# Kernel tuning notes

Measured on AMD Instinct MI355X. Metric: run time of the kernel, lower is better.

## Reference

```python
import jax, jax.numpy as jnp
import numpy as np

K = 60           # output_size (num tags)
START_TAG = 58
STOP_TAG = 59
NEG = -10000.0


def _conv1d(x, w, b, pad):
    # x: (B, Cin, T), w: (Cout, Cin, k) -> (B, Cout, T)
    y = jax.lax.conv_general_dilated(x, w, (1,), [(pad, pad)],
                                     dimension_numbers=('NCH', 'OIH', 'NCH'))
    return y + b[None, :, None]


def _cnn_feats(sentence, w1, b1, w2, b2, w3, b3, w4, b4, w5, b5, fc_w, fc_b):
    # sentence: (T, B, 3) -> (B, 3, T)
    x = jnp.transpose(sentence, (1, 2, 0))
    in2 = jax.nn.relu(_conv1d(x, w1, b1, 1))
    in3 = jax.nn.relu(_conv1d(in2, w2, b2, 1))
    in4 = jax.nn.relu(_conv1d(in3 + in2, w3, b3, 1))
    in5 = jax.nn.relu(_conv1d(in4 + in3, w4, b4, 1))
    c5 = jax.nn.relu(_conv1d(in5 + in4, w5, b5, 2))
    h = jnp.transpose(c5, (2, 0, 1))                 # (T, B, H)
    return jnp.einsum('tbh,kh->tbk', h, fc_w) + fc_b  # (T, B, K)


def _viterbi(feats, trans):
    Bsz = feats.shape[1]
    fv0 = jnp.full((Bsz, K), NEG, dtype=feats.dtype).at[:, START_TAG].set(0.0)

    def step(fv, feat):
        # scores[b, next, prev] = fv[b, prev] + trans[next, prev]
        scores = fv[:, None, :] + trans[None, :, :]
        bptr = jnp.argmax(scores, axis=2)             # (B, K)
        fv_new = jnp.max(scores, axis=2) + feat       # (B, K)
        return fv_new, bptr

    fv, bptrs = jax.lax.scan(step, fv0, feats)        # bptrs: (T, B, K)
    terminal = fv + trans[STOP_TAG]                   # (B, K)
    path_score = jnp.max(terminal, axis=1)            # (B,)
    best_last = jnp.argmax(terminal, axis=1)          # (B,)

    def back(tag, bp):
        prev = jnp.take_along_axis(bp, tag[:, None], axis=1)[:, 0]
        return prev, tag

    _, best_path = jax.lax.scan(back, best_last, bptrs, reverse=True)  # (T, B)
    return path_score, best_path


def setup_inputs() -> dict:
    key = jax.random.key(0)
    ks = jax.random.split(key, 14)
    T, B, HID = 8192, 2, 512

    def u(k, shape, fan_in):
        bound = 1.0 / np.sqrt(fan_in).astype(np.float32)
        return jax.random.uniform(k, shape, minval=-bound, maxval=bound, dtype=jnp.float32)

    sentence = jax.random.normal(ks[0], (T, B, 3), dtype=jnp.float32)
    w1 = u(ks[1], (HID, 3, 3), 3 * 3);      b1 = u(ks[2], (HID,), 3 * 3)
    w2 = u(ks[3], (HID, HID, 3), HID * 3);  b2 = u(ks[4], (HID,), HID * 3)
    w3 = u(ks[5], (HID, HID, 3), HID * 3);  b3 = u(ks[6], (HID,), HID * 3)
    w4 = u(ks[7], (HID, HID, 3), HID * 3);  b4 = u(ks[8], (HID,), HID * 3)
    w5 = u(ks[9], (HID, HID, 5), HID * 5);  b5 = u(ks[10], (HID,), HID * 5)
    fc_w = u(ks[11], (K, HID), HID);        fc_b = u(ks[12], (K,), HID)

    trans = jax.random.normal(ks[13], (K, K), dtype=jnp.float32)
    m = np.zeros((K, K), dtype=bool)
    m[START_TAG, :] = True
    m[:, STOP_TAG] = True
    for i in range(2, K):
        for j in range(2, K):
            if j <= i or j >= i + 2:
                m[j, i] = True
    trans = jnp.where(jnp.asarray(m), jnp.float32(NEG), trans)

    return {'sentence': sentence,
            'w1': w1, 'b1': b1, 'w2': w2, 'b2': b2, 'w3': w3, 'b3': b3,
            'w4': w4, 'b4': b4, 'w5': w5, 'b5': b5,
            'fc_w': fc_w, 'fc_b': fc_b, 'trans': trans}


def reference(sentence, w1, b1, w2, b2, w3, b3, w4, b4, w5, b5, fc_w, fc_b, trans):
    feats = _cnn_feats(sentence, w1, b1, w2, b2, w3, b3, w4, b4, w5, b5, fc_w, fc_b)
    path_score, best_path = _viterbi(feats, trans)
    return path_score, best_path
```

## Files before the change

### kernel.cpp

```cpp
#include <hip/hip_runtime.h>

#define BATCH 2
#define HID 512
#define KTAGS 60
#define NEGV -10000.0f
#define NINF -3.0e38f

template<int CTRL>
__device__ __forceinline__ float dmax(float x) {
    int r = __builtin_amdgcn_update_dpp(__float_as_int(x), __float_as_int(x),
                                        CTRL, 0xf, 0xf, false);
    return fmaxf(x, __int_as_float(r));
}
template<int CTRL>
__device__ __forceinline__ float dmov(float x, float old) {
    int r = __builtin_amdgcn_update_dpp(__float_as_int(old), __float_as_int(x),
                                        CTRL, 0xf, 0xf, false);
    return __int_as_float(r);
}
__device__ __forceinline__ float bfly16max(float x) {
    x = dmax<0xB1>(x);
    x = dmax<0x4E>(x);
    x = dmax<0x141>(x);
    x = dmax<0x140>(x);
    return x;
}

__global__ __launch_bounds__(256) void conv1_kernel(
    const float* __restrict__ sent, const float* __restrict__ w1,
    const float* __restrict__ b1, float* __restrict__ y, int T, int B)
{
    int t = blockIdx.x * 256 + threadIdx.x;
    int c = blockIdx.y;
    int b = blockIdx.z;
    if (t >= T) return;
    float acc = b1[c];
#pragma unroll
    for (int dk = 0; dk < 3; ++dk) {
        int tt = t + dk - 1;
        if (tt >= 0 && tt < T) {
#pragma unroll
            for (int ci = 0; ci < 3; ++ci)
                acc += sent[(size_t)tt * (B * 3) + b * 3 + ci] * w1[c * 9 + ci * 3 + dk];
        }
    }
    y[((size_t)b * HID + c) * T + t] = fmaxf(acc, 0.f);
}

__global__ __launch_bounds__(256) void wtrans_kernel(
    const float* __restrict__ w, float* __restrict__ wt, int K)
{
    int idx = blockIdx.x * 256 + threadIdx.x;
    int total = HID * HID * K;
    if (idx >= total) return;
    int co = idx / (HID * K);
    int rem = idx % (HID * K);
    int ci = rem / K, dk = rem % K;
    wt[((size_t)ci * K + dk) * HID + co] = w[idx];
}

template<int KTAP, bool RES>
__global__ __launch_bounds__(256) void conv_kernel(
    const float* __restrict__ x1, const float* __restrict__ x2,
    const float* __restrict__ wt, const float* __restrict__ bias,
    float* __restrict__ y, int T)
{
    const int PAD = KTAP / 2;
    const int t0 = blockIdx.x * 64;
    const int co0 = blockIdx.y * 128;
    const int b = blockIdx.z;
    __shared__ float Xs[16][72];
    __shared__ float Ws[16][KTAP][128];
    const int tid = threadIdx.x;
    const int tx = tid & 15;
    const int ty = tid >> 4;
    float acc[8][4] = {};
    const size_t plane = (size_t)HID * T;
    const float* xa = x1 + (size_t)b * plane;
    const float* xb = RES ? (x2 + (size_t)b * plane) : nullptr;

    float xr[5];
    float4 wr[2 * KTAP];
    int xci[5], xtt[5];
#pragma unroll
    for (int k = 0; k < 5; ++k) {
        int i = tid + k * 256;
        xci[k] = i / 68;
        xtt[k] = i % 68;
    }

    auto load_stage = [&](int c0) {
#pragma unroll
        for (int k = 0; k < 5; ++k) {
            float v = 0.f;
            if (tid + k * 256 < 16 * 68) {
                int t = t0 + xtt[k] - 2;
                if (t >= 0 && t < T) {
                    size_t off = (size_t)(c0 + xci[k]) * T + t;
                    v = xa[off];
                    if (RES) v += xb[off];
                }
            }
            xr[k] = v;
        }
#pragma unroll
        for (int k = 0; k < 2 * KTAP; ++k) {
            int i = tid + k * 256;
            int c4 = i & 31, r = i >> 5;
            int dk = r % KTAP, ci = r / KTAP;
            wr[k] = *(const float4*)&wt[(((size_t)(c0 + ci) * KTAP + dk) * HID) + co0 + c4 * 4];
        }
    };
    auto write_stage = [&]() {
#pragma unroll
        for (int k = 0; k < 5; ++k)
            if (tid + k * 256 < 16 * 68) Xs[xci[k]][xtt[k]] = xr[k];
#pragma unroll
        for (int k = 0; k < 2 * KTAP; ++k) {
            int i = tid + k * 256;
            int c4 = i & 31, r = i >> 5;
            int dk = r % KTAP, ci = r / KTAP;
            *(float4*)&Ws[ci][dk][c4 * 4] = wr[k];
        }
    };

    load_stage(0);
    for (int c0 = 0; c0 < HID; c0 += 16) {
        write_stage();
        __syncthreads();
        if (c0 + 16 < HID) load_stage(c0 + 16);
#pragma unroll 4
        for (int ci = 0; ci < 16; ++ci) {
            float f8[8];
            *(float4*)&f8[0] = *(const float4*)&Xs[ci][tx * 4];
            *(float4*)&f8[4] = *(const float4*)&Xs[ci][tx * 4 + 4];
#pragma unroll
            for (int dk = 0; dk < KTAP; ++dk) {
                float wv[8];
                *(float4*)&wv[0] = *(const float4*)&Ws[ci][dk][ty * 8];
                *(float4*)&wv[4] = *(const float4*)&Ws[ci][dk][ty * 8 + 4];
#pragma unroll
                for (int r = 0; r < 8; ++r)
#pragma unroll
                    for (int c = 0; c < 4; ++c)
                        acc[r][c] = fmaf(wv[r], f8[c + dk + (2 - PAD)], acc[r][c]);
            }
        }
        __syncthreads();
    }
#pragma unroll
    for (int r = 0; r < 8; ++r) {
        int co = co0 + ty * 8 + r;
        float bv = bias[co];
#pragma unroll
        for (int c = 0; c < 4; ++c) {
            int t = t0 + tx * 4 + c;
            float v = acc[r][c] + bv;
            y[(size_t)b * plane + (size_t)co * T + t] = fmaxf(v, 0.f);
        }
    }
}

__global__ __launch_bounds__(256) void fc_kernel(
    const float* __restrict__ x, const float* __restrict__ fw,
    const float* __restrict__ fb, float* __restrict__ feats, int T)
{
    int t0 = blockIdx.x * 64, b = blockIdx.y;
    __shared__ float Xs[64][65];
    __shared__ float Ws[64][60];
    int tid = threadIdx.x;
    int k = tid & 63, tq = tid >> 6;
    float acc[16] = {};
    const float* xb = x + (size_t)b * HID * T;
    for (int c0 = 0; c0 < HID; c0 += 64) {
        for (int i = tid; i < 64 * 64; i += 256) {
            int ci = i >> 6, tt = i & 63;
            Xs[ci][tt] = xb[(size_t)(c0 + ci) * T + t0 + tt];
        }
        for (int i = tid; i < 64 * 60; i += 256) {
            int kk = i % 60, ci = i / 60;
            Ws[ci][kk] = fw[(size_t)kk * HID + c0 + ci];
        }
        __syncthreads();
        if (k < KTAGS) {
#pragma unroll 8
            for (int ci = 0; ci < 64; ++ci) {
                float wv = Ws[ci][k];
#pragma unroll
                for (int i = 0; i < 16; ++i)
                    acc[i] = fmaf(wv, Xs[ci][tq * 16 + i], acc[i]);
            }
        }
        __syncthreads();
    }
    float bv = (k < KTAGS) ? fb[k] : 0.f;
#pragma unroll
    for (int i = 0; i < 16; ++i) {
        int t = t0 + tq * 16 + i;
        feats[((size_t)t * 2 + b) * 64 + k] = (k < KTAGS) ? acc[i] + bv : NINF;
    }
}

__global__ __launch_bounds__(64) void viterbi_fwd(
    const float* __restrict__ feats, const float* __restrict__ trans,
    float* __restrict__ fvbuf, int T)
{
    const int b = blockIdx.x;
    const int l = threadIdx.x;
    if (l >= 16) return;
    float tc0[4], tc1[4], trc[4], tr0[4], tr1[4], fv[4];
#pragma unroll
    for (int j = 0; j < 4; ++j) {
        int k = 4 * l + j;
        int kc = (k < KTAGS) ? k : (KTAGS - 1);
        bool real = (k < KTAGS);
        tc0[j] = trans[kc * KTAGS + 0];
        tc1[j] = trans[kc * KTAGS + 1];
        trc[j] = (kc >= 1) ? trans[kc * KTAGS + (kc - 1)] : NINF;
        tr0[j] = real ? trans[0 * KTAGS + kc] : NINF;
        tr1[j] = real ? trans[1 * KTAGS + kc] : NINF;
        fv[j]  = real ? ((k == 58) ? 0.f : NEGV) : NINF;
    }
    float fv0h = NEGV, fv1h = NEGV;
    {
        float4 st = {fv[0], fv[1], fv[2], fv[3]};
        *(float4*)&fvbuf[(size_t)b * 64 + 4 * l] = st;
    }
    const float* fp   = feats + b * 64 + 4 * l;
    const float* fp01 = feats + b * 64;
    float* fvp = fvbuf + 128 + b * 64 + 4 * l;

    auto step = [&](float4 f, float2 f01, int j, float* outp) {
        float a0 = fmaxf(fmaxf(fv[0] + tr0[0], fv[1] + tr0[1]), fmaxf(fv[2] + tr0[2], fv[3] + tr0[3]));
        float a1 = fmaxf(fmaxf(fv[0] + tr1[0], fv[1] + tr1[1]), fmaxf(fv[2] + tr1[2], fv[3] + tr1[3]));
        float hi = fmaxf(fv[2], fv[3]);
        float m2 = (l == 0) ? hi : fmaxf(fmaxf(fv[0], fv[1]), hi);
        a0 = bfly16max(a0);
        a1 = bfly16max(a1);
        m2 = bfly16max(m2);
        float p3 = dmov<0x111>(fv[3], fv[3]);
        float bulk = m2 + NEGV;
        float nf0 = a0 + f01.x;
        float nf1 = a1 + f01.y;
        float g0 = fmaxf(fmaxf(fv0h + tc0[0], fv1h + tc1[0]), fmaxf(p3    + trc[0], bulk)) + f.x;
        float g1 = fmaxf(fmaxf(fv0h + tc0[1], fv1h + tc1[1]), fmaxf(fv[0] + trc[1], bulk)) + f.y;
        float g2 = fmaxf(fmaxf(fv0h + tc0[2], fv1h + tc1[2]), fmaxf(fv[1] + trc[2], bulk)) + f.z;
        float g3 = fmaxf(fmaxf(fv0h + tc0[3], fv1h + tc1[3]), fmaxf(fv[2] + trc[3], bulk)) + f.w;
        fv[0] = (l == 0) ? nf0 : g0;
        fv[1] = (l == 0) ? nf1 : g1;
        fv[2] = g2;
        fv[3] = g3;
        fv0h = nf0; fv1h = nf1;
        float4 st = {fv[0], fv[1], fv[2], fv[3]};
        *(float4*)&outp[j * 128] = st;
    };

    float4 fr[8];
    float2 fr2[8];
#pragma unroll
    for (int j = 0; j < 8; ++j) {
        fr[j]  = *(const float4*)&fp[j * 128];
        fr2[j] = *(const float2*)&fp01[j * 128];
    }
    fp += 8 * 128; fp01 += 8 * 128;

    for (int t = 0; t < T; t += 8) {
#pragma unroll
        for (int j = 0; j < 8; ++j) {
            step(fr[j], fr2[j], j, fvp);
            fr[j]  = *(const float4*)&fp[j * 128];
            fr2[j] = *(const float2*)&fp01[j * 128];
        }
        fp += 8 * 128; fp01 += 8 * 128;
        fvp += 8 * 128;
    }
}

__global__ __launch_bounds__(256) void bptr_kernel(
    const float* __restrict__ fvbuf, const float* __restrict__ trans,
    unsigned char* __restrict__ bp, int T)
{
    int b = blockIdx.y;
    int t0 = blockIdx.x * 16;
    __shared__ float trT[KTAGS][64];
    __shared__ float fvs[16][64];
    int tid = threadIdx.x;
    for (int i = tid; i < KTAGS * 64; i += 256) {
        int p = i >> 6, nx = i & 63;
        trT[p][nx] = (nx < KTAGS) ? trans[(size_t)nx * KTAGS + p] : NINF;
    }
    for (int i = tid; i < 16 * 64; i += 256) {
        int w = i >> 6, lx = i & 63;
        fvs[w][lx] = fvbuf[((size_t)(t0 + w) * 2 + b) * 64 + lx];
    }
    __syncthreads();
    int nx = tid & 63, w0 = tid >> 6;
    if (nx < KTAGS) {
#pragma unroll
        for (int j = 0; j < 4; ++j) {
            int w = w0 * 4 + j;
            float m = NINF; int am = 0;
            for (int p = 0; p < KTAGS; ++p) {
                float s = fvs[w][p] + trT[p][nx];
                if (s > m) { m = s; am = p; }
            }
            bp[((size_t)(t0 + w) * 2 + b) * 64 + nx] = (unsigned char)am;
        }
    }
}

__global__ __launch_bounds__(64) void vit_chunkmap(
    const unsigned char* __restrict__ bp, unsigned char* __restrict__ cmap)
{
    int c = blockIdx.x, b = blockIdx.y;
    __shared__ unsigned char bl[128][64];
    int tid = threadIdx.x;
    const unsigned int* src = (const unsigned int*)bp;
    for (int i = tid; i < 128 * 16; i += 64) {
        int row = i >> 4, q = i & 15;
        ((unsigned int*)&bl[row][0])[q] = src[((size_t)(c * 128 + row) * 2 + b) * 16 + q];
    }
    __syncthreads();
    if (tid < KTAGS) {
        int tag = tid;
#pragma unroll 1
        for (int i = 127; i >= 0; --i) tag = bl[i][tag];
        cmap[(c * 2 + b) * 64 + tid] = (unsigned char)tag;
    }
}

__global__ void vit_boundary(const unsigned char* __restrict__ cmap,
                             const float* __restrict__ fvbuf,
                             const float* __restrict__ trans,
                             int* __restrict__ xbound, float* __restrict__ out,
                             int nch, int T)
{
    int b = threadIdx.x;
    if (b < BATCH) {
        const float* fvT = fvbuf + ((size_t)T * 2 + b) * 64;
        float m = NINF; int am = 0;
        for (int p = 0; p < KTAGS; ++p) {
            float s = fvT[p] + trans[59 * KTAGS + p];
            if (s > m) { m = s; am = p; }
        }
        out[b] = m;
        int tag = am;
        for (int c = nch - 1; c >= 0; --c) {
            xbound[c * 2 + b] = tag;
            tag = cmap[(c * 2 + b) * 64 + tag];
        }
    }
}

__global__ __launch_bounds__(64) void vit_emit(
    const unsigned char* __restrict__ bp, const int* __restrict__ xbound,
    float* __restrict__ out)
{
    int c = blockIdx.x, b = blockIdx.y;
    __shared__ unsigned char bl[128][64];
    int tid = threadIdx.x;
    const unsigned int* src = (const unsigned int*)bp;
    for (int i = tid; i < 128 * 16; i += 64) {
        int row = i >> 4, q = i & 15;
        ((unsigned int*)&bl[row][0])[q] = src[((size_t)(c * 128 + row) * 2 + b) * 16 + q];
    }
    __syncthreads();
    if (tid == 0) {
        int tag = xbound[c * 2 + b];
        for (int i = 127; i >= 0; --i) {
            out[2 + (size_t)(c * 128 + i) * 2 + b] = (float)tag;
            tag = bl[i][tag];
        }
    }
}

extern "C" void kernel_launch(void* const* d_in, const int* in_sizes, int n_in,
                              void* d_out, int out_size, void* d_ws, size_t ws_size,
                              hipStream_t stream) {
    const float* sent = (const float*)d_in[0];
    const float* w1 = (const float*)d_in[1];  const float* b1 = (const float*)d_in[2];
    const float* w2 = (const float*)d_in[3];  const float* b2 = (const float*)d_in[4];
    const float* w3 = (const float*)d_in[5];  const float* b3 = (const float*)d_in[6];
    const float* w4 = (const float*)d_in[7];  const float* b4 = (const float*)d_in[8];
    const float* w5 = (const float*)d_in[9];  const float* b5 = (const float*)d_in[10];
    const float* fw = (const float*)d_in[11]; const float* fb = (const float*)d_in[12];
    const float* trans = (const float*)d_in[13];

    const int B = BATCH;
    const int T = in_sizes[0] / (B * 3);

    char* ws = (char*)d_ws;
    const size_t SZBUF = (size_t)2 * HID * 8192 * 4;
    float* bufA = (float*)(ws);
    float* bufB = (float*)(ws + SZBUF);
    float* bufC = (float*)(ws + 2 * SZBUF);
    float* wslot = (float*)(ws + 3 * SZBUF);
    float* feats = wslot;
    float* fvbuf = bufC;
    unsigned char* bp = (unsigned char*)ws;
    unsigned char* cmap = (unsigned char*)(ws + 2 * 1024 * 1024);
    int* xbound = (int*)(ws + 3 * 1024 * 1024);
    float* outp = (float*)d_out;

    conv1_kernel<<<dim3(T / 256, HID, B), 256, 0, stream>>>(sent, w1, b1, bufA, T, B);

    wtrans_kernel<<<(HID * HID * 3 + 255) / 256, 256, 0, stream>>>(w2, wslot, 3);
    conv_kernel<3, false><<<dim3(T / 64, HID / 128, B), 256, 0, stream>>>(bufA, nullptr, wslot, b2, bufB, T);
    wtrans_kernel<<<(HID * HID * 3 + 255) / 256, 256, 0, stream>>>(w3, wslot, 3);
    conv_kernel<3, true ><<<dim3(T / 64, HID / 128, B), 256, 0, stream>>>(bufB, bufA, wslot, b3, bufC, T);
    wtrans_kernel<<<(HID * HID * 3 + 255) / 256, 256, 0, stream>>>(w4, wslot, 3);
    conv_kernel<3, true ><<<dim3(T / 64, HID / 128, B), 256, 0, stream>>>(bufC, bufB, wslot, b4, bufA, T);
    wtrans_kernel<<<(HID * HID * 5 + 255) / 256, 256, 0, stream>>>(w5, wslot, 5);
    conv_kernel<5, true ><<<dim3(T / 64, HID / 128, B), 256, 0, stream>>>(bufA, bufC, wslot, b5, bufB, T);

    fc_kernel<<<dim3(T / 64, B), 256, 0, stream>>>(bufB, fw, fb, feats, T);

    viterbi_fwd<<<dim3(B), 64, 0, stream>>>(feats, trans, fvbuf, T);
    bptr_kernel<<<dim3(T / 16, B), 256, 0, stream>>>(fvbuf, trans, bp, T);
    vit_chunkmap<<<dim3(T / 128, B), 64, 0, stream>>>(bp, cmap);
    vit_boundary<<<dim3(1), 64, 0, stream>>>(cmap, fvbuf, trans, xbound, outp, T / 128, T);
    vit_emit<<<dim3(T / 128, B), 64, 0, stream>>>(bp, xbound, outp);
}
```

Measured before the change: 4.183 ms.

## Add producer warp to Viterbi forward and halve conv channel tile

The serial Viterbi forward recurrence now runs in a 128-thread block. One wavefront computes the recurrence from LDS while a second wavefront prefetches the next 32 timesteps of features into a double-buffered ring and writes the previous block's forward scores back to global memory. The aim is to take global load and store latency off the serial dependency chain, at the cost of a block barrier every 32 steps. Separately, the conv kernel's input-channel tile drops from 16 to 8 with a full unroll, which cuts LDS use and registers but doubles the number of loop iterations and barriers.

```diff
diff --git a/kernel.cpp b/kernel.cpp
--- a/kernel.cpp
+++ b/kernel.cpp
@@ -5,6 +5,7 @@
 #define KTAGS 60
 #define NEGV -10000.0f
 #define NINF -3.0e38f
+#define VBLK 32
 
 template<int CTRL>
 __device__ __forceinline__ float dmax(float x) {
@@ -69,8 +70,8 @@
     const int t0 = blockIdx.x * 64;
     const int co0 = blockIdx.y * 128;
     const int b = blockIdx.z;
-    __shared__ float Xs[16][72];
-    __shared__ float Ws[16][KTAP][128];
+    __shared__ float Xs[8][72];
+    __shared__ float Ws[8][KTAP][128];
     const int tid = threadIdx.x;
     const int tx = tid & 15;
     const int ty = tid >> 4;
@@ -79,11 +80,11 @@
     const float* xa = x1 + (size_t)b * plane;
     const float* xb = RES ? (x2 + (size_t)b * plane) : nullptr;
 
-    float xr[5];
-    float4 wr[2 * KTAP];
-    int xci[5], xtt[5];
-#pragma unroll
-    for (int k = 0; k < 5; ++k) {
+    float xr[3];
+    float4 wr[KTAP];
+    int xci[3], xtt[3];
+#pragma unroll
+    for (int k = 0; k < 3; ++k) {
         int i = tid + k * 256;
         xci[k] = i / 68;
         xtt[k] = i % 68;
@@ -91,9 +92,9 @@
 
     auto load_stage = [&](int c0) {
 #pragma unroll
-        for (int k = 0; k < 5; ++k) {
+        for (int k = 0; k < 3; ++k) {
             float v = 0.f;
-            if (tid + k * 256 < 16 * 68) {
+            if (tid + k * 256 < 8 * 68) {
                 int t = t0 + xtt[k] - 2;
                 if (t >= 0 && t < T) {
                     size_t off = (size_t)(c0 + xci[k]) * T + t;
@@ -104,7 +105,7 @@
             xr[k] = v;
         }
 #pragma unroll
-        for (int k = 0; k < 2 * KTAP; ++k) {
+        for (int k = 0; k < KTAP; ++k) {
             int i = tid + k * 256;
             int c4 = i & 31, r = i >> 5;
             int dk = r % KTAP, ci = r / KTAP;
@@ -113,10 +114,10 @@
     };
     auto write_stage = [&]() {
 #pragma unroll
-        for (int k = 0; k < 5; ++k)
-            if (tid + k * 256 < 16 * 68) Xs[xci[k]][xtt[k]] = xr[k];
-#pragma unroll
-        for (int k = 0; k < 2 * KTAP; ++k) {
+        for (int k = 0; k < 3; ++k)
+            if (tid + k * 256 < 8 * 68) Xs[xci[k]][xtt[k]] = xr[k];
+#pragma unroll
+        for (int k = 0; k < KTAP; ++k) {
             int i = tid + k * 256;
             int c4 = i & 31, r = i >> 5;
             int dk = r % KTAP, ci = r / KTAP;
@@ -125,12 +126,12 @@
     };
 
     load_stage(0);
-    for (int c0 = 0; c0 < HID; c0 += 16) {
+    for (int c0 = 0; c0 < HID; c0 += 8) {
         write_stage();
         __syncthreads();
-        if (c0 + 16 < HID) load_stage(c0 + 16);
-#pragma unroll 4
-        for (int ci = 0; ci < 16; ++ci) {
+        if (c0 + 8 < HID) load_stage(c0 + 8);
+#pragma unroll
+        for (int ci = 0; ci < 8; ++ci) {
             float f8[8];
             *(float4*)&f8[0] = *(const float4*)&Xs[ci][tx * 4];
             *(float4*)&f8[4] = *(const float4*)&Xs[ci][tx * 4 + 4];
@@ -201,78 +202,105 @@
     }
 }
 
-__global__ __launch_bounds__(64) void viterbi_fwd(
+__global__ __launch_bounds__(128) void viterbi_fwd(
     const float* __restrict__ feats, const float* __restrict__ trans,
     float* __restrict__ fvbuf, int T)
 {
     const int b = blockIdx.x;
-    const int l = threadIdx.x;
-    if (l >= 16) return;
+    const int tid = threadIdx.x;
+    const int wv = tid >> 6;
+    const int l = tid & 63;
+    __shared__ float fring[2][VBLK][64];
+    __shared__ float fvring[2][VBLK][64];
+    const int NB = T / VBLK;
+
     float tc0[4], tc1[4], trc[4], tr0[4], tr1[4], fv[4];
-#pragma unroll
-    for (int j = 0; j < 4; ++j) {
-        int k = 4 * l + j;
-        int kc = (k < KTAGS) ? k : (KTAGS - 1);
-        bool real = (k < KTAGS);
-        tc0[j] = trans[kc * KTAGS + 0];
-        tc1[j] = trans[kc * KTAGS + 1];
-        trc[j] = (kc >= 1) ? trans[kc * KTAGS + (kc - 1)] : NINF;
-        tr0[j] = real ? trans[0 * KTAGS + kc] : NINF;
-        tr1[j] = real ? trans[1 * KTAGS + kc] : NINF;
-        fv[j]  = real ? ((k == 58) ? 0.f : NEGV) : NINF;
-    }
     float fv0h = NEGV, fv1h = NEGV;
-    {
+    if (wv == 0 && l < 16) {
+#pragma unroll
+        for (int j = 0; j < 4; ++j) {
+            int k = 4 * l + j;
+            int kc = (k < KTAGS) ? k : (KTAGS - 1);
+            bool real = (k < KTAGS);
+            tc0[j] = trans[kc * KTAGS + 0];
+            tc1[j] = trans[kc * KTAGS + 1];
+            trc[j] = (kc >= 1) ? trans[kc * KTAGS + (kc - 1)] : NINF;
+            tr0[j] = real ? trans[0 * KTAGS + kc] : NINF;
+            tr1[j] = real ? trans[1 * KTAGS + kc] : NINF;
+            fv[j]  = real ? ((k == 58) ? 0.f : NEGV) : NINF;
+        }
         float4 st = {fv[0], fv[1], fv[2], fv[3]};
         *(float4*)&fvbuf[(size_t)b * 64 + 4 * l] = st;
-    }
-    const float* fp   = feats + b * 64 + 4 * l;
-    const float* fp01 = feats + b * 64;
-    float* fvp = fvbuf + 128 + b * 64 + 4 * l;
-
-    auto step = [&](float4 f, float2 f01, int j, float* outp) {
-        float a0 = fmaxf(fmaxf(fv[0] + tr0[0], fv[1] + tr0[1]), fmaxf(fv[2] + tr0[2], fv[3] + tr0[3]));
-        float a1 = fmaxf(fmaxf(fv[0] + tr1[0], fv[1] + tr1[1]), fmaxf(fv[2] + tr1[2], fv[3] + tr1[3]));
-        float hi = fmaxf(fv[2], fv[3]);
-        float m2 = (l == 0) ? hi : fmaxf(fmaxf(fv[0], fv[1]), hi);
-        a0 = bfly16max(a0);
-        a1 = bfly16max(a1);
-        m2 = bfly16max(m2);
-        float p3 = dmov<0x111>(fv[3], fv[3]);
-        float bulk = m2 + NEGV;
-        float nf0 = a0 + f01.x;
-        float nf1 = a1 + f01.y;
-        float g0 = fmaxf(fmaxf(fv0h + tc0[0], fv1h + tc1[0]), fmaxf(p3    + trc[0], bulk)) + f.x;
-        float g1 = fmaxf(fmaxf(fv0h + tc0[1], fv1h + tc1[1]), fmaxf(fv[0] + trc[1], bulk)) + f.y;
-        float g2 = fmaxf(fmaxf(fv0h + tc0[2], fv1h + tc1[2]), fmaxf(fv[1] + trc[2], bulk)) + f.z;
-        float g3 = fmaxf(fmaxf(fv0h + tc0[3], fv1h + tc1[3]), fmaxf(fv[2] + trc[3], bulk)) + f.w;
-        fv[0] = (l == 0) ? nf0 : g0;
-        fv[1] = (l == 0) ? nf1 : g1;
-        fv[2] = g2;
-        fv[3] = g3;
-        fv0h = nf0; fv1h = nf1;
-        float4 st = {fv[0], fv[1], fv[2], fv[3]};
-        *(float4*)&outp[j * 128] = st;
-    };
-
-    float4 fr[8];
-    float2 fr2[8];
-#pragma unroll
-    for (int j = 0; j < 8; ++j) {
-        fr[j]  = *(const float4*)&fp[j * 128];
-        fr2[j] = *(const float2*)&fp01[j * 128];
-    }
-    fp += 8 * 128; fp01 += 8 * 128;
-
-    for (int t = 0; t < T; t += 8) {
-#pragma unroll
-        for (int j = 0; j < 8; ++j) {
-            step(fr[j], fr2[j], j, fvp);
-            fr[j]  = *(const float4*)&fp[j * 128];
-            fr2[j] = *(const float2*)&fp01[j * 128];
-        }
-        fp += 8 * 128; fp01 += 8 * 128;
-        fvp += 8 * 128;
+    } else if (wv == 1) {
+        for (int i = l; i < VBLK * 16; i += 64) {
+            int j = i >> 4, k4 = i & 15;
+            float4 v = *(const float4*)&feats[(size_t)j * 128 + b * 64 + k4 * 4];
+            *(float4*)&fring[0][j][k4 * 4] = v;
+        }
+    }
+    __syncthreads();
+
+    for (int k = 0; k < NB; ++k) {
+        const int cur = k & 1;
+        if (wv == 0) {
+            if (l < 16) {
+#pragma unroll
+                for (int j = 0; j < VBLK; ++j) {
+                    float4 f = *(const float4*)&fring[cur][j][4 * l];
+                    float2 f01 = *(const float2*)&fring[cur][j][0];
+                    float a0 = fmaxf(fmaxf(fv[0] + tr0[0], fv[1] + tr0[1]),
+                                     fmaxf(fv[2] + tr0[2], fv[3] + tr0[3]));
+                    float a1 = fmaxf(fmaxf(fv[0] + tr1[0], fv[1] + tr1[1]),
+                                     fmaxf(fv[2] + tr1[2], fv[3] + tr1[3]));
+                    float hi = fmaxf(fv[2], fv[3]);
+                    float m2 = (l == 0) ? hi : fmaxf(fmaxf(fv[0], fv[1]), hi);
+                    m2 = m2 + NEGV;
+                    a0 = bfly16max(a0);
+                    a1 = bfly16max(a1);
+                    float bulk = bfly16max(m2);
+                    float p3 = dmov<0x111>(fv[3], fv[3]);
+                    float nf0 = a0 + f01.x;
+                    float nf1 = a1 + f01.y;
+                    float g0 = fmaxf(fmaxf(fv0h + tc0[0], fv1h + tc1[0]), fmaxf(p3    + trc[0], bulk)) + f.x;
+                    float g1 = fmaxf(fmaxf(fv0h + tc0[1], fv1h + tc1[1]), fmaxf(fv[0] + trc[1], bulk)) + f.y;
+                    float g2 = fmaxf(fmaxf(fv0h + tc0[2], fv1h + tc1[2]), fmaxf(fv[1] + trc[2], bulk)) + f.z;
+                    float g3 = fmaxf(fmaxf(fv0h + tc0[3], fv1h + tc1[3]), fmaxf(fv[2] + trc[3], bulk)) + f.w;
+                    fv[0] = (l == 0) ? nf0 : g0;
+                    fv[1] = (l == 0) ? nf1 : g1;
+                    fv[2] = g2;
+                    fv[3] = g3;
+                    fv0h = nf0; fv1h = nf1;
+                    float4 st = {fv[0], fv[1], fv[2], fv[3]};
+                    *(float4*)&fvring[cur][j][4 * l] = st;
+                }
+            }
+        } else {
+            if (k + 1 < NB) {
+                int t0 = (k + 1) * VBLK;
+                for (int i = l; i < VBLK * 16; i += 64) {
+                    int j = i >> 4, k4 = i & 15;
+                    float4 v = *(const float4*)&feats[(size_t)(t0 + j) * 128 + b * 64 + k4 * 4];
+                    *(float4*)&fring[(k + 1) & 1][j][k4 * 4] = v;
+                }
+            }
+            if (k > 0) {
+                int t0 = (k - 1) * VBLK + 1;
+                for (int i = l; i < VBLK * 16; i += 64) {
+                    int j = i >> 4, k4 = i & 15;
+                    float4 v = *(const float4*)&fvring[(k + 1) & 1][j][k4 * 4];
+                    *(float4*)&fvbuf[(size_t)(t0 + j) * 128 + b * 64 + k4 * 4] = v;
+                }
+            }
+        }
+        __syncthreads();
+    }
+    if (wv == 1) {
+        int t0 = (NB - 1) * VBLK + 1;
+        for (int i = l; i < VBLK * 16; i += 64) {
+            int j = i >> 4, k4 = i & 15;
+            float4 v = *(const float4*)&fvring[(NB - 1) & 1][j][k4 * 4];
+            *(float4*)&fvbuf[(size_t)(t0 + j) * 128 + b * 64 + k4 * 4] = v;
+        }
     }
 }
 
@@ -415,7 +443,7 @@
 
     fc_kernel<<<dim3(T / 64, B), 256, 0, stream>>>(bufB, fw, fb, feats, T);
 
-    viterbi_fwd<<<dim3(B), 64, 0, stream>>>(feats, trans, fvbuf, T);
+    viterbi_fwd<<<dim3(B), 128, 0, stream>>>(feats, trans, fvbuf, T);
     bptr_kernel<<<dim3(T / 16, B), 256, 0, stream>>>(fvbuf, trans, bp, T);
     vit_chunkmap<<<dim3(T / 128, B), 64, 0, stream>>>(bp, cmap);
     vit_boundary<<<dim3(1), 64, 0, stream>>>(cmap, fvbuf, trans, xbound, outp, T / 128, T);
```

After: 4.446 ms. 1.06x slower.
